# Optimization experiments

Measured on AMD Instinct MI355X. Metric: run time of the kernel, lower is better.

Reference implementation:

```python
import jax, jax.numpy as jnp
import numpy as np

B, C, NP, DM, H, TOPK = 16, 1024, 512, 512, 8, 16
D = DM // H  # d_head = 64


def _topk_mask(scores, k):
    """Binary mask keeping top-k entries per last-dim row. scores: (..., C)."""
    shape = scores.shape
    c = shape[-1]
    k = min(k, c)
    _, idx = jax.lax.top_k(scores, k)            # (..., k)
    flat = scores.reshape(-1, c)
    idxf = idx.reshape(-1, k)
    rows = jnp.arange(flat.shape[0])[:, None]
    mask = jnp.zeros_like(flat).at[rows, idxf].set(1.0)
    return mask.reshape(shape)


def setup_inputs() -> dict:
    key = jax.random.key(0)
    ks = jax.random.split(key, 7)
    M = jax.random.normal(ks[0], (B, C, NP), dtype=jnp.float32)
    s_in = 1.0 / np.sqrt(NP)
    Wq = jax.random.uniform(ks[1], (DM, NP), jnp.float32, -s_in, s_in)
    Wk = jax.random.uniform(ks[2], (DM, NP), jnp.float32, -s_in, s_in)
    Wv = jax.random.uniform(ks[3], (DM, NP), jnp.float32, -s_in, s_in)
    s_out = 1.0 / np.sqrt(DM)
    Wo = jax.random.uniform(ks[4], (NP, DM), jnp.float32, -s_out, s_out)
    bo = jax.random.uniform(ks[5], (NP,), jnp.float32, -s_out, s_out)
    gate = jnp.asarray(1.0, dtype=jnp.float32)
    return {"M": M, "Wq": Wq, "Wk": Wk, "Wv": Wv, "Wo": Wo, "bo": bo, "gate": gate}


def reference(M, Wq, Wk, Wv, Wo, bo, gate):
    # projections: torch Linear(no bias) -> M @ W.T
    def proj(W):
        x = jnp.einsum('bcn,dn->bcd', M, W)          # (B, C, DM)
        return x.reshape(B, C, H, D).transpose(0, 2, 1, 3)  # (B, H, C, D)

    q, k, v = proj(Wq), proj(Wk), proj(Wv)
    scale = D ** -0.5
    scores = jnp.einsum('bhid,bhjd->bhij', q, k) * scale     # (B, H, C, C)

    sparse_mask = jax.lax.stop_gradient(_topk_mask(scores, TOPK))
    neg_inf = jnp.finfo(scores.dtype).min
    masked = jnp.where(sparse_mask == 0, neg_inf, scores)
    attn = jnp.nan_to_num(jax.nn.softmax(masked, axis=-1))

    out = jnp.einsum('bhij,bhjd->bhid', attn, v)             # (B, H, C, D)
    out = out.transpose(0, 2, 1, 3).reshape(B, C, DM)        # (B, C, DM)
    delta = out @ Wo.T + bo                                  # (B, C, NP); dropout is eval-mode identity
    M_tilde = M + gate * delta

    avg_scores = scores.mean(axis=1)                         # (B, C, C)
    A = _topk_mask(avg_scores, TOPK)
    return M_tilde, A
```

## Files before the change

kernel.cpp:

```cpp
#include <hip/hip_runtime.h>
#include <hip/hip_bf16.h>

#define B_  16
#define C_  1024
#define NP_ 512
#define DM_ 512
#define H_  8
#define D_  64
#define BC_ 16384

#define PAVG_STRIDE 17
#define NBMAX 4
#define FLDS 40
#define FLDS2 72
#define STR_C 132

typedef unsigned long long ull;
typedef unsigned short u16;
using short8 = __attribute__((ext_vector_type(8))) short;
using half8  = __attribute__((ext_vector_type(8))) _Float16;
using f32x4  = __attribute__((ext_vector_type(4))) float;

__device__ __forceinline__ u16 f2bf(float x) {
    __hip_bfloat16 h = __float2bfloat16(x);
    return *reinterpret_cast<u16*>(&h);
}
__device__ __forceinline__ float bf2f(u16 v) {
    return __uint_as_float(((unsigned)v) << 16);
}
__device__ __forceinline__ u16 h_bits(_Float16 h) {
    return *reinterpret_cast<u16*>(&h);
}


__device__ __forceinline__ void hsplit_stage(const u16* __restrict__ Ah, const u16* __restrict__ Al,
    const u16* __restrict__ Bh, const u16* __restrict__ Bl,
    int lda, int ldb, int row0, int col0, int k0,
    u16* __restrict__ sAh, u16* __restrict__ sAl,
    u16* __restrict__ sBh, u16* __restrict__ sBl, int tid)
{
#pragma unroll
    for (int rep = 0; rep < 2; ++rep) {
        const int c = tid + rep * 256;
        const int row = c >> 2, kq = (c & 3) * 8;
        const size_t ga = (size_t)(row0 + row) * lda + k0 + kq;
        const size_t gb = (size_t)(col0 + row) * ldb + k0 + kq;
        *(uint4*)(&sAh[row * FLDS + kq]) = *(const uint4*)(Ah + ga);
        *(uint4*)(&sAl[row * FLDS + kq]) = *(const uint4*)(Al + ga);
        *(uint4*)(&sBh[row * FLDS + kq]) = *(const uint4*)(Bh + gb);
        *(uint4*)(&sBl[row * FLDS + kq]) = *(const uint4*)(Bl + gb);
    }
}

__device__ __forceinline__ void hsplit_compute(const u16* __restrict__ sAh, const u16* __restrict__ sAl,
    const u16* __restrict__ sBh, const u16* __restrict__ sBl,
    int lane, int wm, int wn, f32x4 (&acc)[4][4])
{
    const int q8 = (lane >> 4) * 8, l16 = lane & 15;
    half8 bh[4], bl_[4];
#pragma unroll
    for (int nt = 0; nt < 4; ++nt) {
        const int o = (wn * 64 + nt * 16 + l16) * FLDS + q8;
        bh[nt]  = *(const half8*)(&sBh[o]);
        bl_[nt] = *(const half8*)(&sBl[o]);
    }
#pragma unroll
    for (int mt = 0; mt < 4; ++mt) {
        const int o = (wm * 64 + mt * 16 + l16) * FLDS + q8;
        const half8 ah = *(const half8*)(&sAh[o]);
        const half8 al = *(const half8*)(&sAl[o]);
#pragma unroll
        for (int nt = 0; nt < 4; ++nt) {
            acc[mt][nt] = __builtin_amdgcn_mfma_f32_16x16x32_f16(ah, bh[nt],  acc[mt][nt], 0, 0, 0);
            acc[mt][nt] = __builtin_amdgcn_mfma_f32_16x16x32_f16(al, bh[nt],  acc[mt][nt], 0, 0, 0);
            acc[mt][nt] = __builtin_amdgcn_mfma_f32_16x16x32_f16(ah, bl_[nt], acc[mt][nt], 0, 0, 0);
            acc[mt][nt] = __builtin_amdgcn_mfma_f32_16x16x32_f16(al, bl_[nt], acc[mt][nt], 0, 0, 0);
        }
    }
}


__global__ __launch_bounds__(256) void w_convert(
    const float* __restrict__ Wo, const float* __restrict__ Wv,
    const float* __restrict__ Wq, const float* __restrict__ Wk,
    u16* __restrict__ Wob, u16* __restrict__ Wvb,
    u16* __restrict__ Wqh, u16* __restrict__ Wql,
    u16* __restrict__ Wkh, u16* __restrict__ Wkl)
{
    const int i = (blockIdx.x * 256 + threadIdx.x) * 4;
    const int y = blockIdx.y;
    if (y < 2) {
        const float* X = (y == 0) ? Wo : Wv;
        u16* Dp = (y == 0) ? Wob : Wvb;
        const float4 v = *(const float4*)(X + i);
        ushort4 o;
        o.x = f2bf(v.x); o.y = f2bf(v.y); o.z = f2bf(v.z); o.w = f2bf(v.w);
        *(ushort4*)(Dp + i) = o;
    } else {
        const float* X = (y == 2) ? Wq : Wk;
        u16* Hh = (y == 2) ? Wqh : Wkh;
        u16* Hl = (y == 2) ? Wql : Wkl;
        const float4 v = *(const float4*)(X + i);
        ushort4 oh, ol;
        {
            _Float16 h = (_Float16)v.x; oh.x = h_bits(h); ol.x = h_bits((_Float16)(v.x - (float)h));
        }{
            _Float16 h = (_Float16)v.y; oh.y = h_bits(h); ol.y = h_bits((_Float16)(v.y - (float)h));
        }{
            _Float16 h = (_Float16)v.z; oh.z = h_bits(h); ol.z = h_bits((_Float16)(v.z - (float)h));
        }{
            _Float16 h = (_Float16)v.w; oh.w = h_bits(h); ol.w = h_bits((_Float16)(v.w - (float)h));
        }
        *(ushort4*)(Hh + i) = oh;
        *(ushort4*)(Hl + i) = ol;
    }
}

__global__ __launch_bounds__(256) void mi_convert(const float* __restrict__ X,
    u16* __restrict__ Bb, u16* __restrict__ Hh, u16* __restrict__ Hl)
{
    const int i = (blockIdx.x * 256 + threadIdx.x) * 4;
    const float4 v = *(const float4*)(X + i);
    ushort4 ob, oh, ol;
    {
        _Float16 h = (_Float16)v.x; ob.x = f2bf(v.x); oh.x = h_bits(h); ol.x = h_bits((_Float16)(v.x - (float)h));
    }{
        _Float16 h = (_Float16)v.y; ob.y = f2bf(v.y); oh.y = h_bits(h); ol.y = h_bits((_Float16)(v.y - (float)h));
    }{
        _Float16 h = (_Float16)v.z; ob.z = f2bf(v.z); oh.z = h_bits(h); ol.z = h_bits((_Float16)(v.z - (float)h));
    }{
        _Float16 h = (_Float16)v.w; ob.w = f2bf(v.w); oh.w = h_bits(h); ol.w = h_bits((_Float16)(v.w - (float)h));
    }
    *(ushort4*)(Bb + i) = ob;
    *(ushort4*)(Hh + i) = oh;
    *(ushort4*)(Hl + i) = ol;
}

__global__ __launch_bounds__(256) void qk_gemm_mfma(
    const u16* __restrict__ Mih, const u16* __restrict__ Mil,
    const u16* __restrict__ Wqh, const u16* __restrict__ Wql,
    const u16* __restrict__ Wkh, const u16* __restrict__ Wkl,
    u16* __restrict__ Qh, u16* __restrict__ Ql,
    u16* __restrict__ Kh, u16* __restrict__ Kl)
{
    __shared__ u16 sAh[128 * FLDS];
    __shared__ u16 sAl[128 * FLDS];
    __shared__ u16 sBh[128 * FLDS];
    __shared__ u16 sBl[128 * FLDS];

    const int tid = threadIdx.x, lane = tid & 63, w = tid >> 6;
    const int wm = w >> 1, wn = w & 1;
    const int z = blockIdx.z;
    const u16* Bh = z ? Wkh : Wqh;
    const u16* Bl = z ? Wkl : Wql;
    u16* outH = z ? Kh : Qh;
    u16* outL = z ? Kl : Ql;
    const int row0 = blockIdx.x * 128, col0 = blockIdx.y * 128;

    f32x4 acc[4][4];
#pragma unroll
    for (int mt = 0; mt < 4; ++mt)
#pragma unroll
        for (int nt = 0; nt < 4; ++nt)
            acc[mt][nt] = (f32x4){0.f, 0.f, 0.f, 0.f};

    for (int k0 = 0; k0 < NP_; k0 += 32) {
        hsplit_stage(Mih, Mil, Bh, Bl, NP_, NP_, row0, col0, k0, sAh, sAl, sBh, sBl, tid);
        __syncthreads();
        hsplit_compute(sAh, sAl, sBh, sBl, lane, wm, wn, acc);
        __syncthreads();
    }

    const int quad = lane >> 4, l16 = lane & 15;
#pragma unroll
    for (int mt = 0; mt < 4; ++mt)
#pragma unroll
        for (int nt = 0; nt < 4; ++nt) {
            const int n = col0 + wn * 64 + nt * 16 + l16;
            const int hh = n >> 6, dd = n & 63;
#pragma unroll
            for (int reg = 0; reg < 4; ++reg) {
                const int m = row0 + wm * 64 + mt * 16 + quad * 4 + reg;
                const int bl = m >> 10, c = m & 1023;
                const size_t idx = ((size_t)(bl * 8 + hh) * C_ + c) * D_ + dd;
                const float v = acc[mt][nt][reg];
                const _Float16 vh = (_Float16)v;
                outH[idx] = h_bits(vh);
                outL[idx] = h_bits((_Float16)(v - (float)vh));
            }
        }
}

__global__ __launch_bounds__(256) void score_gemm_mfma(
    const u16* __restrict__ Qh, const u16* __restrict__ Ql,
    const u16* __restrict__ Kh, const u16* __restrict__ Kl,
    float* __restrict__ S)
{
    __shared__ u16 smem[4 * 128 * FLDS2];
    u16* sAh = smem;
    u16* sAl = smem + 128 * FLDS2;
    u16* sBh = smem + 2 * 128 * FLDS2;
    u16* sBl = smem + 3 * 128 * FLDS2;

    const int tid = threadIdx.x, lane = tid & 63, w = tid >> 6;
    const int wm = w >> 1, wn = w & 1;
    const int z = blockIdx.z;
    const size_t off = (size_t)z * C_ * D_;
    const u16* Ah = Qh + off;  const u16* Al = Ql + off;
    const u16* Bh = Kh + off;  const u16* Bl = Kl + off;
    float* Cp = S + (size_t)z * C_ * C_;
    const int row0 = blockIdx.x * 128, col0 = blockIdx.y * 128;

    f32x4 acc[4][4];
#pragma unroll
    for (int mt = 0; mt < 4; ++mt)
#pragma unroll
        for (int nt = 0; nt < 4; ++nt)
            acc[mt][nt] = (f32x4){0.f, 0.f, 0.f, 0.f};

#pragma unroll
    for (int rep = 0; rep < 4; ++rep) {
        const int c = tid + rep * 256;
        const int row = c >> 3, kq = (c & 7) * 8;
        const size_t ga = (size_t)(row0 + row) * D_ + kq;
        const size_t gb = (size_t)(col0 + row) * D_ + kq;
        *(uint4*)(&sAh[row * FLDS2 + kq]) = *(const uint4*)(Ah + ga);
        *(uint4*)(&sAl[row * FLDS2 + kq]) = *(const uint4*)(Al + ga);
        *(uint4*)(&sBh[row * FLDS2 + kq]) = *(const uint4*)(Bh + gb);
        *(uint4*)(&sBl[row * FLDS2 + kq]) = *(const uint4*)(Bl + gb);
    }
    __syncthreads();

    const int q8 = (lane >> 4) * 8, l16 = lane & 15;
#pragma unroll
    for (int ks = 0; ks < 2; ++ks) {
        const int kof = ks * 32 + q8;
        half8 bh[4], bl_[4];
#pragma unroll
        for (int nt = 0; nt < 4; ++nt) {
            const int o = (wn * 64 + nt * 16 + l16) * FLDS2 + kof;
            bh[nt]  = *(const half8*)(&sBh[o]);
            bl_[nt] = *(const half8*)(&sBl[o]);
        }
#pragma unroll
        for (int mt = 0; mt < 4; ++mt) {
            const int o = (wm * 64 + mt * 16 + l16) * FLDS2 + kof;
            const half8 ah = *(const half8*)(&sAh[o]);
            const half8 al = *(const half8*)(&sAl[o]);
#pragma unroll
            for (int nt = 0; nt < 4; ++nt) {
                acc[mt][nt] = __builtin_amdgcn_mfma_f32_16x16x32_f16(ah, bh[nt],  acc[mt][nt], 0, 0, 0);
                acc[mt][nt] = __builtin_amdgcn_mfma_f32_16x16x32_f16(al, bh[nt],  acc[mt][nt], 0, 0, 0);
                acc[mt][nt] = __builtin_amdgcn_mfma_f32_16x16x32_f16(ah, bl_[nt], acc[mt][nt], 0, 0, 0);
                acc[mt][nt] = __builtin_amdgcn_mfma_f32_16x16x32_f16(al, bl_[nt], acc[mt][nt], 0, 0, 0);
            }
        }
    }

    __syncthreads();
    float* st = (float*)smem;
    const int quad = lane >> 4;
#pragma unroll
    for (int mt = 0; mt < 4; ++mt)
#pragma unroll
        for (int nt = 0; nt < 4; ++nt) {
            const int n = wn * 64 + nt * 16 + l16;
#pragma unroll
            for (int reg = 0; reg < 4; ++reg) {
                const int m = wm * 64 + mt * 16 + quad * 4 + reg;
                st[m * STR_C + n] = acc[mt][nt][reg] * 0.125f;
            }
        }
    __syncthreads();
#pragma unroll
    for (int pass = 0; pass < 16; ++pass) {
        const int idx = pass * 256 + tid;
        const int row = idx >> 5;
        const int c4  = (idx & 31) << 2;
        const float4 v = *(const float4*)&st[row * STR_C + c4];
        *(float4*)(Cp + (size_t)(row0 + row) * C_ + col0 + c4) = v;
    }
}

__global__ __launch_bounds__(256) void v_gemm_mfma(const u16* __restrict__ Mib,
    const u16* __restrict__ Wvb, u16* __restrict__ Vb)
{
    __shared__ u16 As[128 * FLDS];
    __shared__ u16 Bs[128 * FLDS];
    const int tid = threadIdx.x, lane = tid & 63, w = tid >> 6;
    const int wm = w >> 1, wn = w & 1;
    const int row0 = blockIdx.x * 128, col0 = blockIdx.y * 128;

    f32x4 acc[4][4];
#pragma unroll
    for (int mt = 0; mt < 4; ++mt)
#pragma unroll
        for (int nt = 0; nt < 4; ++nt)
            acc[mt][nt] = (f32x4){0.f, 0.f, 0.f, 0.f};

    const int q8 = (lane >> 4) * 8, l16 = lane & 15;
    for (int k0 = 0; k0 < NP_; k0 += 32) {
#pragma unroll
        for (int rep = 0; rep < 2; ++rep) {
            const int c = tid + rep * 256;
            const int row = c >> 2, kq = (c & 3) * 8;
            *(uint4*)(&As[row * FLDS + kq]) = *(const uint4*)(Mib + (size_t)(row0 + row) * NP_ + k0 + kq);
            *(uint4*)(&Bs[row * FLDS + kq]) = *(const uint4*)(Wvb + (size_t)(col0 + row) * NP_ + k0 + kq);
        }
        __syncthreads();
        short8 a[4], bfr[4];
#pragma unroll
        for (int mt = 0; mt < 4; ++mt)
            a[mt] = *(const short8*)(&As[(wm * 64 + mt * 16 + l16) * FLDS + q8]);
#pragma unroll
        for (int nt = 0; nt < 4; ++nt)
            bfr[nt] = *(const short8*)(&Bs[(wn * 64 + nt * 16 + l16) * FLDS + q8]);
#pragma unroll
        for (int mt = 0; mt < 4; ++mt)
#pragma unroll
            for (int nt = 0; nt < 4; ++nt)
                acc[mt][nt] = __builtin_amdgcn_mfma_f32_16x16x32_bf16(a[mt], bfr[nt], acc[mt][nt], 0, 0, 0);
        __syncthreads();
    }
    const int quad = lane >> 4;
#pragma unroll
    for (int mt = 0; mt < 4; ++mt)
#pragma unroll
        for (int nt = 0; nt < 4; ++nt) {
            const int n = col0 + wn * 64 + nt * 16 + l16;
#pragma unroll
            for (int reg = 0; reg < 4; ++reg) {
                const int m = row0 + wm * 64 + mt * 16 + quad * 4 + reg;
                Vb[(size_t)m * DM_ + n] = f2bf(acc[mt][nt][reg]);
            }
        }
}


__device__ __forceinline__ ull pack1(float f, int j) {
    unsigned b = __float_as_uint(f);
    unsigned u = b ^ ((unsigned)((int)b >> 31) | 0x80000000u);
    return ((ull)u << 32) | (unsigned)(1023 - j);
}
__device__ __forceinline__ float unpack_val(ull e) {
    unsigned u = (unsigned)(e >> 32);
    unsigned b = u ^ ((u & 0x80000000u) ? 0x80000000u : 0xFFFFFFFFu);
    return __uint_as_float(b);
}
__device__ __forceinline__ int unpack_j(ull e) {
    return 1023 - (int)(e & 0xFFFFFFFFu);
}
__device__ __forceinline__ unsigned mono32(float f) {
    unsigned b = __float_as_uint(f);
    return b ^ ((unsigned)((int)b >> 31) | 0x80000000u);
}
__device__ __forceinline__ float mono32_inv(unsigned u) {
    unsigned b = u ^ ((u & 0x80000000u) ? 0x80000000u : 0xFFFFFFFFu);
    return __uint_as_float(b);
}

__device__ __forceinline__ unsigned radix16_u32(unsigned k)
{
    unsigned p = 0u;
#pragma unroll
    for (int b = 31; b >= 12; --b) {
        const unsigned t = p | (1u << b);
        if (__popcll(__ballot(k >= t)) >= 16) p = t;
    }
    return p;
}

__device__ __forceinline__ void radix16_dual_u32(unsigned kA, unsigned kB,
                                                 unsigned &pA, unsigned &pB)
{
    pA = 0u; pB = 0u;
#pragma unroll
    for (int b = 31; b >= 12; --b) {
        const unsigned tA = pA | (1u << b);
        const unsigned tB = pB | (1u << b);
        const ull mA = __ballot(kA >= tA);
        const ull mB = __ballot(kB >= tB);
        if (__popcll(mA) >= 16) pA = tA;
        if (__popcll(mB) >= 16) pB = tB;
    }
}

__device__ __forceinline__ void topk16_fast(float (&f)[16], const int lane,
                                            ull* candw, ull (&out)[16])
{
    float mv = f[0];
#pragma unroll
    for (int r = 1; r < 16; ++r) mv = fmaxf(mv, f[r]);
    const float tau = mono32_inv(radix16_u32(mono32(mv)));

    unsigned msk = 0u;
#pragma unroll
    for (int r = 0; r < 16; ++r) msk |= (f[r] >= tau) ? (1u << r) : 0u;
    const int cnt = __popc(msk);
    int incl = cnt;
#pragma unroll
    for (int off = 1; off < 64; off <<= 1) {
        const int t = __shfl_up(incl, off);
        incl += (lane >= off) ? t : 0;
    }
    const int total = __shfl(incl, 63);

    if (total <= 64) {
        int ofs = incl - cnt;
        unsigned m = msk;
        while (m) {
            const int r = __ffs(m) - 1;
            m &= m - 1;
            candw[ofs++] = pack1(f[r], (lane << 4) + r);
        }
        ull e = candw[lane];
        if (lane >= total) e = 0ull;
        if (total <= 32) {
#pragma unroll
            for (int k = 2; k <= 32; k <<= 1) {
#pragma unroll
                for (int j = k >> 1; j > 0; j >>= 1) {
                    const ull p = __shfl_xor(e, j);
                    const bool kmax = ((lane & k) == 0) == ((lane & j) == 0);
                    if ((p > e) == kmax) e = p;
                }
            }
        } else {
#pragma unroll
            for (int k = 2; k <= 64; k <<= 1) {
#pragma unroll
                for (int j = k >> 1; j > 0; j >>= 1) {
                    const ull p = __shfl_xor(e, j);
                    const bool kmax = ((lane & k) == 0) == ((lane & j) == 0);
                    if ((p > e) == kmax) e = p;
                }
            }
        }
#pragma unroll
        for (int t = 0; t < 16; ++t) out[t] = __shfl(e, t);
    } else {
        for (int it = 0; it < 16; ++it) {
            float bv = f[0]; int bj = lane << 4;
#pragma unroll
            for (int r = 1; r < 16; ++r)
                if (f[r] > bv) { bv = f[r]; bj = (lane << 4) + r; }
#pragma unroll
            for (int off = 32; off >= 1; off >>= 1) {
                const float ov = __shfl_xor(bv, off);
                const int   oj = __shfl_xor(bj, off);
                if (ov > bv || (ov == bv && oj < bj)) { bv = ov; bj = oj; }
            }
            out[it] = pack1(bv, bj);
            if ((bj >> 4) == lane) f[bj & 15] = -3.402823466e38f;
        }
    }
}

__device__ __forceinline__ ull topk16_serial(float (&f)[16], const int lane)
{
    ull e = 0ull;
    for (int it = 0; it < 16; ++it) {
        float bv = f[0]; int bj = lane << 4;
#pragma unroll
        for (int r = 1; r < 16; ++r)
            if (f[r] > bv) { bv = f[r]; bj = (lane << 4) + r; }
#pragma unroll
        for (int off = 32; off >= 1; off >>= 1) {
            const float ov = __shfl_xor(bv, off);
            const int   oj = __shfl_xor(bj, off);
            if (ov > bv || (ov == bv && oj < bj)) { bv = ov; bj = oj; }
        }
        if (lane == it) e = pack1(bv, bj);
        if ((bj >> 4) == lane) f[bj & 15] = -3.402823466e38f;
    }
    return e;
}

__device__ __forceinline__ void topk16_dual(float (&fA)[16], float (&fB)[16],
                                            const int lane, ull* cwA, ull* cwB,
                                            ull &eA, ull &eB)
{
    float mA = fA[0], mB = fB[0];
#pragma unroll
    for (int r = 1; r < 16; ++r) { mA = fmaxf(mA, fA[r]); mB = fmaxf(mB, fB[r]); }
    unsigned pA, pB;
    radix16_dual_u32(mono32(mA), mono32(mB), pA, pB);
    const float tauA = mono32_inv(pA);
    const float tauB = mono32_inv(pB);

    unsigned mskA = 0u, mskB = 0u;
#pragma unroll
    for (int r = 0; r < 16; ++r) {
        mskA |= (fA[r] >= tauA) ? (1u << r) : 0u;
        mskB |= (fB[r] >= tauB) ? (1u << r) : 0u;
    }
    const int cntA = __popc(mskA), cntB = __popc(mskB);
    int inclA = cntA, inclB = cntB;
#pragma unroll
    for (int off = 1; off < 64; off <<= 1) {
        const int tA = __shfl_up(inclA, off);
        const int tB = __shfl_up(inclB, off);
        inclA += (lane >= off) ? tA : 0;
        inclB += (lane >= off) ? tB : 0;
    }
    const int totalA = __shfl(inclA, 63);
    const int totalB = __shfl(inclB, 63);

    if (totalA <= 64) {
        int ofs = inclA - cntA;
        unsigned m = mskA;
        while (m) {
            const int r = __ffs(m) - 1;
            m &= m - 1;
            cwA[ofs++] = pack1(fA[r], (lane << 4) + r);
        }
    }
    if (totalB <= 64) {
        int ofs = inclB - cntB;
        unsigned m = mskB;
        while (m) {
            const int r = __ffs(m) - 1;
            m &= m - 1;
            cwB[ofs++] = pack1(fB[r], (lane << 4) + r);
        }
    }
    eA = (totalA <= 64 && lane < totalA) ? cwA[lane] : 0ull;
    eB = (totalB <= 64 && lane < totalB) ? cwB[lane] : 0ull;
    if (totalA <= 32 && totalB <= 32) {
#pragma unroll
        for (int k = 2; k <= 32; k <<= 1) {
#pragma unroll
            for (int j = k >> 1; j > 0; j >>= 1) {
                const ull pAx = __shfl_xor(eA, j);
                const ull pBx = __shfl_xor(eB, j);
                const bool kmax = ((lane & k) == 0) == ((lane & j) == 0);
                if ((pAx > eA) == kmax) eA = pAx;
                if ((pBx > eB) == kmax) eB = pBx;
            }
        }
    } else {
#pragma unroll
        for (int k = 2; k <= 64; k <<= 1) {
#pragma unroll
            for (int j = k >> 1; j > 0; j >>= 1) {
                const ull pAx = __shfl_xor(eA, j);
                const ull pBx = __shfl_xor(eB, j);
                const bool kmax = ((lane & k) == 0) == ((lane & j) == 0);
                if ((pAx > eA) == kmax) eA = pAx;
                if ((pBx > eB) == kmax) eB = pBx;
            }
        }
    }
    if (totalA > 64) eA = topk16_serial(fA, lane);
    if (totalB > 64) eB = topk16_serial(fB, lane);
}

__device__ __forceinline__ void attn_out(const ull e, const u16* __restrict__ V,
                                         int bl, int i, int h, int lane,
                                         u16* __restrict__ O)
{
    float vals[16]; int jl[16];
#pragma unroll
    for (int t = 0; t < 16; ++t) {
        const ull et = __shfl(e, t);
        vals[t] = unpack_val(et);
        jl[t]   = unpack_j(et);
    }
    const float mx = vals[0];
    float wv[16];
    float Z = 0.0f;
#pragma unroll
    for (int t = 0; t < 16; ++t) { wv[t] = __expf(vals[t] - mx); Z += wv[t]; }
    const float inv = 1.0f / Z;
#pragma unroll
    for (int t = 0; t < 16; ++t) wv[t] *= inv;
    float o = 0.0f;
#pragma unroll
    for (int t = 0; t < 16; ++t)
        o = fmaf(wv[t], bf2f(V[((size_t)(bl * C_ + jl[t])) * DM_ + h * D_ + lane]), o);
    O[((size_t)(bl * C_ + i)) * DM_ + h * D_ + lane] = f2bf(o);
}

__global__ __launch_bounds__(320) void topk_attn(const float* __restrict__ S,
    const u16* __restrict__ V, u16* __restrict__ O,
    float* __restrict__ Aout, int b0)
{
    __shared__ float pavg[4 * 64 * PAVG_STRIDE];
    __shared__ ull   cand[4][2][64];
    __shared__ ull   candA[64];

    const int tid = threadIdx.x, lane = tid & 63, w = tid >> 6;
    const int rb = blockIdx.x, bl = rb >> 10, i = rb & 1023;
    const int b = b0 + bl;

    float f1[16], f2[16];
    if (w < 4) {
        const float* r1 = S + ((size_t)(bl * 8 + w) * C_ + i) * C_ + lane * 16;
        const float* r2 = S + ((size_t)(bl * 8 + w + 4) * C_ + i) * C_ + lane * 16;
#pragma unroll
        for (int q = 0; q < 4; ++q) {
            const float4 x = *(const float4*)(r1 + q * 4);
            f1[q * 4 + 0] = x.x; f1[q * 4 + 1] = x.y; f1[q * 4 + 2] = x.z; f1[q * 4 + 3] = x.w;
            const float4 y = *(const float4*)(r2 + q * 4);
            f2[q * 4 + 0] = y.x; f2[q * 4 + 1] = y.y; f2[q * 4 + 2] = y.z; f2[q * 4 + 3] = y.w;
        }
        float* pw = pavg + w * 64 * PAVG_STRIDE + lane * PAVG_STRIDE;
#pragma unroll
        for (int r = 0; r < 16; ++r) pw[r] = f1[r] + f2[r];
    }
    __syncthreads();

    if (w < 4) {
        ull eA, eB;
        topk16_dual(f1, f2, lane, cand[w][0], cand[w][1], eA, eB);
        attn_out(eA, V, bl, i, w,     lane, O);
        attn_out(eB, V, bl, i, w + 4, lane, O);
    } else {
        float fa[16];
#pragma unroll
        for (int r = 0; r < 16; ++r) {
            fa[r] = pavg[0 * 64 * PAVG_STRIDE + lane * PAVG_STRIDE + r]
                  + pavg[1 * 64 * PAVG_STRIDE + lane * PAVG_STRIDE + r]
                  + pavg[2 * 64 * PAVG_STRIDE + lane * PAVG_STRIDE + r]
                  + pavg[3 * 64 * PAVG_STRIDE + lane * PAVG_STRIDE + r];
        }
        ull top[16];
        topk16_fast(fa, lane, candA, top);
        unsigned mybits = 0u;
#pragma unroll
        for (int t = 0; t < 16; ++t) {
            const int j = unpack_j(top[t]);
            if ((j >> 4) == lane) mybits |= 1u << (j & 15);
        }
        float* arow = Aout + ((size_t)(b * C_ + i)) * C_ + lane * 16;
#pragma unroll
        for (int q = 0; q < 4; ++q) {
            float4 o4;
            o4.x = ((mybits >> (q * 4 + 0)) & 1u) ? 1.0f : 0.0f;
            o4.y = ((mybits >> (q * 4 + 1)) & 1u) ? 1.0f : 0.0f;
            o4.z = ((mybits >> (q * 4 + 2)) & 1u) ? 1.0f : 0.0f;
            o4.w = ((mybits >> (q * 4 + 3)) & 1u) ? 1.0f : 0.0f;
            *(float4*)(arow + q * 4) = o4;
        }
    }
}

__global__ __launch_bounds__(256) void final_gemm_mfma(const u16* __restrict__ O,
    const u16* __restrict__ Wob, const float* __restrict__ Mi,
    const float* __restrict__ bo, const float* __restrict__ gatep,
    float* __restrict__ out)
{
    __shared__ u16 As[128 * FLDS];
    __shared__ u16 Bs[128 * FLDS];
    const int tid = threadIdx.x, lane = tid & 63, w = tid >> 6;
    const int wm = w >> 1, wn = w & 1;
    const int row0 = blockIdx.x * 128, col0 = blockIdx.y * 128;

    f32x4 acc[4][4];
#pragma unroll
    for (int mt = 0; mt < 4; ++mt)
#pragma unroll
        for (int nt = 0; nt < 4; ++nt)
            acc[mt][nt] = (f32x4){0.f, 0.f, 0.f, 0.f};

    const int q8 = (lane >> 4) * 8, l16 = lane & 15;
    for (int k0 = 0; k0 < DM_; k0 += 32) {
#pragma unroll
        for (int rep = 0; rep < 2; ++rep) {
            const int c = tid + rep * 256;
            const int row = c >> 2, kq = (c & 3) * 8;
            *(uint4*)(&As[row * FLDS + kq]) = *(const uint4*)(O   + (size_t)(row0 + row) * DM_ + k0 + kq);
            *(uint4*)(&Bs[row * FLDS + kq]) = *(const uint4*)(Wob + (size_t)(col0 + row) * DM_ + k0 + kq);
        }
        __syncthreads();
        short8 a[4], bfr[4];
#pragma unroll
        for (int mt = 0; mt < 4; ++mt)
            a[mt] = *(const short8*)(&As[(wm * 64 + mt * 16 + l16) * FLDS + q8]);
#pragma unroll
        for (int nt = 0; nt < 4; ++nt)
            bfr[nt] = *(const short8*)(&Bs[(wn * 64 + nt * 16 + l16) * FLDS + q8]);
#pragma unroll
        for (int mt = 0; mt < 4; ++mt)
#pragma unroll
            for (int nt = 0; nt < 4; ++nt)
                acc[mt][nt] = __builtin_amdgcn_mfma_f32_16x16x32_bf16(a[mt], bfr[nt], acc[mt][nt], 0, 0, 0);
        __syncthreads();
    }

    const float g = gatep[0];
    const int quad = lane >> 4;
#pragma unroll
    for (int mt = 0; mt < 4; ++mt) {
#pragma unroll
        for (int nt = 0; nt < 4; ++nt) {
            const int n = col0 + wn * 64 + nt * 16 + l16;
            const float bon = bo[n];
#pragma unroll
            for (int reg = 0; reg < 4; ++reg) {
                const int m = row0 + wm * 64 + mt * 16 + quad * 4 + reg;
                out[(size_t)m * NP_ + n] = Mi[(size_t)m * NP_ + n] + g * (acc[mt][nt][reg] + bon);
            }
        }
    }
}

extern "C" void kernel_launch(void* const* d_in, const int* in_sizes, int n_in,
                              void* d_out, int out_size, void* d_ws, size_t ws_size,
                              hipStream_t stream)
{
    (void)in_sizes; (void)n_in; (void)out_size;
    const float* Mi   = (const float*)d_in[0];
    const float* Wq   = (const float*)d_in[1];
    const float* Wk   = (const float*)d_in[2];
    const float* Wv   = (const float*)d_in[3];
    const float* Wo   = (const float*)d_in[4];
    const float* bo   = (const float*)d_in[5];
    const float* gate = (const float*)d_in[6];
    float* out  = (float*)d_out;
    float* Aout = out + (size_t)BC_ * NP_;

    char* p = (char*)d_ws;
    const size_t SZ_W   = (size_t)NP_ * DM_ * 2;
    const size_t SZ_BIG = (size_t)BC_ * DM_ * 2;
    u16* Wob = (u16*)p; p += SZ_W;
    u16* Wvb = (u16*)p; p += SZ_W;
    u16* Wqh = (u16*)p; p += SZ_W;
    u16* Wql = (u16*)p; p += SZ_W;
    u16* Wkh = (u16*)p; p += SZ_W;
    u16* Wkl = (u16*)p; p += SZ_W;
    u16* Mib = (u16*)p; p += SZ_BIG;
    u16* Mih = (u16*)p; p += SZ_BIG;
    u16* Mil = (u16*)p; p += SZ_BIG;
    u16* Qh  = (u16*)p; p += SZ_BIG;
    u16* Ql  = (u16*)p; p += SZ_BIG;
    u16* Kh  = (u16*)p; p += SZ_BIG;
    u16* Kl  = (u16*)p; p += SZ_BIG;
    u16* Vb  = (u16*)p; p += SZ_BIG;
    u16* Of  = (u16*)p; p += SZ_BIG;
    float* Sc = (float*)p;

    const size_t fixed = 6 * SZ_W + 9 * SZ_BIG;
    const size_t chunk_bytes = (size_t)H_ * C_ * C_ * 4;
    size_t availB = (ws_size > fixed) ? (ws_size - fixed) : 0;
    int NB = (int)(availB / chunk_bytes);
    if (NB < 1) NB = 1;
    if (NB > NBMAX) NB = NBMAX;

    w_convert<<<dim3(NP_ * DM_ / 1024, 4), 256, 0, stream>>>(
        Wo, Wv, Wq, Wk, Wob, Wvb, Wqh, Wql, Wkh, Wkl);
    mi_convert<<<dim3((int)((size_t)BC_ * NP_ / 1024)), 256, 0, stream>>>(Mi, Mib, Mih, Mil);

    qk_gemm_mfma<<<dim3(BC_ / 128, DM_ / 128, 2), 256, 0, stream>>>(
        Mih, Mil, Wqh, Wql, Wkh, Wkl, Qh, Ql, Kh, Kl);
    v_gemm_mfma<<<dim3(BC_ / 128, DM_ / 128), 256, 0, stream>>>(Mib, Wvb, Vb);

    for (int b0 = 0; b0 < B_; b0 += NB) {
        const int nb = (B_ - b0 < NB) ? (B_ - b0) : NB;
        const size_t hoff = (size_t)b0 * H_ * C_ * D_;
        score_gemm_mfma<<<dim3(C_ / 128, C_ / 128, nb * 8), 256, 0, stream>>>(
            Qh + hoff, Ql + hoff, Kh + hoff, Kl + hoff, Sc);
        topk_attn<<<dim3(nb * C_), 320, 0, stream>>>(
            Sc, Vb + (size_t)b0 * C_ * DM_, Of + (size_t)b0 * C_ * DM_, Aout, b0);
    }

    final_gemm_mfma<<<dim3(BC_ / 128, NP_ / 128), 256, 0, stream>>>(
        Of, Wob, Mi, bo, gate, out);
}
```

Before: 599.3 us.

## Use one wavefront per head in topk_attn instead of dual-row waves

The top-k attention kernel now launches 9 wavefronts per row block (8 heads plus one for the averaged mask) instead of 5, with each head wave running a single-row top-k rather than the interleaved dual-row routine. The head-sum reduction moves entirely into the averaging wave, which now reads eight LDS slices. The softmax in attn_out is also restructured to avoid per-lane register arrays. This raises parallelism per block and shortens the per-wave dependency chain, at the cost of larger blocks, more LDS and less instruction-level parallelism within each wave.

```diff
diff --git a/kernel.cpp b/kernel.cpp
--- a/kernel.cpp
+++ b/kernel.cpp
@@ -347,6 +347,10 @@
     unsigned b = u ^ ((u & 0x80000000u) ? 0x80000000u : 0xFFFFFFFFu);
     return __uint_as_float(b);
 }
+__device__ __forceinline__ float unpack_val_u32(unsigned u) {
+    unsigned b = u ^ ((u & 0x80000000u) ? 0x80000000u : 0xFFFFFFFFu);
+    return __uint_as_float(b);
+}
 __device__ __forceinline__ int unpack_j(ull e) {
     return 1023 - (int)(e & 0xFFFFFFFFu);
 }
@@ -370,23 +374,27 @@
     return p;
 }
 
-__device__ __forceinline__ void radix16_dual_u32(unsigned kA, unsigned kB,
-                                                 unsigned &pA, unsigned &pB)
-{
-    pA = 0u; pB = 0u;
-#pragma unroll
-    for (int b = 31; b >= 12; --b) {
-        const unsigned tA = pA | (1u << b);
-        const unsigned tB = pB | (1u << b);
-        const ull mA = __ballot(kA >= tA);
-        const ull mB = __ballot(kB >= tB);
-        if (__popcll(mA) >= 16) pA = tA;
-        if (__popcll(mB) >= 16) pB = tB;
-    }
-}
-
-__device__ __forceinline__ void topk16_fast(float (&f)[16], const int lane,
-                                            ull* candw, ull (&out)[16])
+__device__ __forceinline__ ull topk16_serial(float (&f)[16], const int lane)
+{
+    ull e = 0ull;
+    for (int it = 0; it < 16; ++it) {
+        float bv = f[0]; int bj = lane << 4;
+#pragma unroll
+        for (int r = 1; r < 16; ++r)
+            if (f[r] > bv) { bv = f[r]; bj = (lane << 4) + r; }
+#pragma unroll
+        for (int off = 32; off >= 1; off >>= 1) {
+            const float ov = __shfl_xor(bv, off);
+            const int   oj = __shfl_xor(bj, off);
+            if (ov > bv || (ov == bv && oj < bj)) { bv = ov; bj = oj; }
+        }
+        if (lane == it) e = pack1(bv, bj);
+        if ((bj >> 4) == lane) f[bj & 15] = -3.402823466e38f;
+    }
+    return e;
+}
+
+__device__ __forceinline__ ull topk16_single(float (&f)[16], const int lane, ull* candw)
 {
     float mv = f[0];
 #pragma unroll
@@ -413,8 +421,7 @@
             m &= m - 1;
             candw[ofs++] = pack1(f[r], (lane << 4) + r);
         }
-        ull e = candw[lane];
-        if (lane >= total) e = 0ull;
+        ull e = (lane < total) ? candw[lane] : 0ull;
         if (total <= 32) {
 #pragma unroll
             for (int k = 2; k <= 32; k <<= 1) {
@@ -436,200 +443,76 @@
                 }
             }
         }
-#pragma unroll
-        for (int t = 0; t < 16; ++t) out[t] = __shfl(e, t);
-    } else {
-        for (int it = 0; it < 16; ++it) {
-            float bv = f[0]; int bj = lane << 4;
-#pragma unroll
-            for (int r = 1; r < 16; ++r)
-                if (f[r] > bv) { bv = f[r]; bj = (lane << 4) + r; }
-#pragma unroll
-            for (int off = 32; off >= 1; off >>= 1) {
-                const float ov = __shfl_xor(bv, off);
-                const int   oj = __shfl_xor(bj, off);
-                if (ov > bv || (ov == bv && oj < bj)) { bv = ov; bj = oj; }
-            }
-            out[it] = pack1(bv, bj);
-            if ((bj >> 4) == lane) f[bj & 15] = -3.402823466e38f;
-        }
-    }
-}
-
-__device__ __forceinline__ ull topk16_serial(float (&f)[16], const int lane)
-{
-    ull e = 0ull;
-    for (int it = 0; it < 16; ++it) {
-        float bv = f[0]; int bj = lane << 4;
-#pragma unroll
-        for (int r = 1; r < 16; ++r)
-            if (f[r] > bv) { bv = f[r]; bj = (lane << 4) + r; }
-#pragma unroll
-        for (int off = 32; off >= 1; off >>= 1) {
-            const float ov = __shfl_xor(bv, off);
-            const int   oj = __shfl_xor(bj, off);
-            if (ov > bv || (ov == bv && oj < bj)) { bv = ov; bj = oj; }
-        }
-        if (lane == it) e = pack1(bv, bj);
-        if ((bj >> 4) == lane) f[bj & 15] = -3.402823466e38f;
-    }
-    return e;
-}
-
-__device__ __forceinline__ void topk16_dual(float (&fA)[16], float (&fB)[16],
-                                            const int lane, ull* cwA, ull* cwB,
-                                            ull &eA, ull &eB)
-{
-    float mA = fA[0], mB = fB[0];
-#pragma unroll
-    for (int r = 1; r < 16; ++r) { mA = fmaxf(mA, fA[r]); mB = fmaxf(mB, fB[r]); }
-    unsigned pA, pB;
-    radix16_dual_u32(mono32(mA), mono32(mB), pA, pB);
-    const float tauA = mono32_inv(pA);
-    const float tauB = mono32_inv(pB);
-
-    unsigned mskA = 0u, mskB = 0u;
-#pragma unroll
-    for (int r = 0; r < 16; ++r) {
-        mskA |= (fA[r] >= tauA) ? (1u << r) : 0u;
-        mskB |= (fB[r] >= tauB) ? (1u << r) : 0u;
-    }
-    const int cntA = __popc(mskA), cntB = __popc(mskB);
-    int inclA = cntA, inclB = cntB;
-#pragma unroll
-    for (int off = 1; off < 64; off <<= 1) {
-        const int tA = __shfl_up(inclA, off);
-        const int tB = __shfl_up(inclB, off);
-        inclA += (lane >= off) ? tA : 0;
-        inclB += (lane >= off) ? tB : 0;
-    }
-    const int totalA = __shfl(inclA, 63);
-    const int totalB = __shfl(inclB, 63);
-
-    if (totalA <= 64) {
-        int ofs = inclA - cntA;
-        unsigned m = mskA;
-        while (m) {
-            const int r = __ffs(m) - 1;
-            m &= m - 1;
-            cwA[ofs++] = pack1(fA[r], (lane << 4) + r);
-        }
-    }
-    if (totalB <= 64) {
-        int ofs = inclB - cntB;
-        unsigned m = mskB;
-        while (m) {
-            const int r = __ffs(m) - 1;
-            m &= m - 1;
-            cwB[ofs++] = pack1(fB[r], (lane << 4) + r);
-        }
-    }
-    eA = (totalA <= 64 && lane < totalA) ? cwA[lane] : 0ull;
-    eB = (totalB <= 64 && lane < totalB) ? cwB[lane] : 0ull;
-    if (totalA <= 32 && totalB <= 32) {
-#pragma unroll
-        for (int k = 2; k <= 32; k <<= 1) {
-#pragma unroll
-            for (int j = k >> 1; j > 0; j >>= 1) {
-                const ull pAx = __shfl_xor(eA, j);
-                const ull pBx = __shfl_xor(eB, j);
-                const bool kmax = ((lane & k) == 0) == ((lane & j) == 0);
-                if ((pAx > eA) == kmax) eA = pAx;
-                if ((pBx > eB) == kmax) eB = pBx;
-            }
-        }
-    } else {
-#pragma unroll
-        for (int k = 2; k <= 64; k <<= 1) {
-#pragma unroll
-            for (int j = k >> 1; j > 0; j >>= 1) {
-                const ull pAx = __shfl_xor(eA, j);
-                const ull pBx = __shfl_xor(eB, j);
-                const bool kmax = ((lane & k) == 0) == ((lane & j) == 0);
-                if ((pAx > eA) == kmax) eA = pAx;
-                if ((pBx > eB) == kmax) eB = pBx;
-            }
-        }
-    }
-    if (totalA > 64) eA = topk16_serial(fA, lane);
-    if (totalB > 64) eB = topk16_serial(fB, lane);
+        return e;
+    }
+    return topk16_serial(f, lane);
 }
 
 __device__ __forceinline__ void attn_out(const ull e, const u16* __restrict__ V,
                                          int bl, int i, int h, int lane,
                                          u16* __restrict__ O)
 {
-    float vals[16]; int jl[16];
+    const int ehi = (int)(unsigned)(e >> 32);
+    const float mx = unpack_val_u32((unsigned)__shfl(ehi, 0));
+    float Z = 0.0f;
+#pragma unroll
+    for (int t = 0; t < 16; ++t)
+        Z += __expf(unpack_val_u32((unsigned)__shfl(ehi, t)) - mx);
+    const float inv = 1.0f / Z;
+    float o = 0.0f;
 #pragma unroll
     for (int t = 0; t < 16; ++t) {
         const ull et = __shfl(e, t);
-        vals[t] = unpack_val(et);
-        jl[t]   = unpack_j(et);
-    }
-    const float mx = vals[0];
-    float wv[16];
-    float Z = 0.0f;
-#pragma unroll
-    for (int t = 0; t < 16; ++t) { wv[t] = __expf(vals[t] - mx); Z += wv[t]; }
-    const float inv = 1.0f / Z;
-#pragma unroll
-    for (int t = 0; t < 16; ++t) wv[t] *= inv;
-    float o = 0.0f;
-#pragma unroll
-    for (int t = 0; t < 16; ++t)
-        o = fmaf(wv[t], bf2f(V[((size_t)(bl * C_ + jl[t])) * DM_ + h * D_ + lane]), o);
+        const float wv = __expf(unpack_val(et) - mx) * inv;
+        o = fmaf(wv, bf2f(V[((size_t)(bl * C_ + unpack_j(et))) * DM_ + h * D_ + lane]), o);
+    }
     O[((size_t)(bl * C_ + i)) * DM_ + h * D_ + lane] = f2bf(o);
 }
 
-__global__ __launch_bounds__(320) void topk_attn(const float* __restrict__ S,
+__global__ __launch_bounds__(576) void topk_attn(const float* __restrict__ S,
     const u16* __restrict__ V, u16* __restrict__ O,
     float* __restrict__ Aout, int b0)
 {
-    __shared__ float pavg[4 * 64 * PAVG_STRIDE];
-    __shared__ ull   cand[4][2][64];
-    __shared__ ull   candA[64];
+    __shared__ float pavg[8 * 64 * PAVG_STRIDE];
+    __shared__ ull   cand[9][64];
 
     const int tid = threadIdx.x, lane = tid & 63, w = tid >> 6;
     const int rb = blockIdx.x, bl = rb >> 10, i = rb & 1023;
     const int b = b0 + bl;
 
-    float f1[16], f2[16];
-    if (w < 4) {
+    float f[16];
+    if (w < 8) {
         const float* r1 = S + ((size_t)(bl * 8 + w) * C_ + i) * C_ + lane * 16;
-        const float* r2 = S + ((size_t)(bl * 8 + w + 4) * C_ + i) * C_ + lane * 16;
 #pragma unroll
         for (int q = 0; q < 4; ++q) {
             const float4 x = *(const float4*)(r1 + q * 4);
-            f1[q * 4 + 0] = x.x; f1[q * 4 + 1] = x.y; f1[q * 4 + 2] = x.z; f1[q * 4 + 3] = x.w;
-            const float4 y = *(const float4*)(r2 + q * 4);
-            f2[q * 4 + 0] = y.x; f2[q * 4 + 1] = y.y; f2[q * 4 + 2] = y.z; f2[q * 4 + 3] = y.w;
+            f[q * 4 + 0] = x.x; f[q * 4 + 1] = x.y; f[q * 4 + 2] = x.z; f[q * 4 + 3] = x.w;
         }
         float* pw = pavg + w * 64 * PAVG_STRIDE + lane * PAVG_STRIDE;
 #pragma unroll
-        for (int r = 0; r < 16; ++r) pw[r] = f1[r] + f2[r];
+        for (int r = 0; r < 16; ++r) pw[r] = f[r];
     }
     __syncthreads();
 
-    if (w < 4) {
-        ull eA, eB;
-        topk16_dual(f1, f2, lane, cand[w][0], cand[w][1], eA, eB);
-        attn_out(eA, V, bl, i, w,     lane, O);
-        attn_out(eB, V, bl, i, w + 4, lane, O);
+    if (w < 8) {
+        const ull e = topk16_single(f, lane, cand[w]);
+        attn_out(e, V, bl, i, w, lane, O);
     } else {
         float fa[16];
 #pragma unroll
         for (int r = 0; r < 16; ++r) {
-            fa[r] = pavg[0 * 64 * PAVG_STRIDE + lane * PAVG_STRIDE + r]
-                  + pavg[1 * 64 * PAVG_STRIDE + lane * PAVG_STRIDE + r]
-                  + pavg[2 * 64 * PAVG_STRIDE + lane * PAVG_STRIDE + r]
-                  + pavg[3 * 64 * PAVG_STRIDE + lane * PAVG_STRIDE + r];
-        }
-        ull top[16];
-        topk16_fast(fa, lane, candA, top);
+            const int o = lane * PAVG_STRIDE + r;
+            const float t0 = pavg[0 * 64 * PAVG_STRIDE + o] + pavg[4 * 64 * PAVG_STRIDE + o];
+            const float t1 = pavg[1 * 64 * PAVG_STRIDE + o] + pavg[5 * 64 * PAVG_STRIDE + o];
+            const float t2 = pavg[2 * 64 * PAVG_STRIDE + o] + pavg[6 * 64 * PAVG_STRIDE + o];
+            const float t3 = pavg[3 * 64 * PAVG_STRIDE + o] + pavg[7 * 64 * PAVG_STRIDE + o];
+            fa[r] = ((t0 + t1) + t2) + t3;
+        }
+        const ull e = topk16_single(fa, lane, cand[8]);
         unsigned mybits = 0u;
 #pragma unroll
         for (int t = 0; t < 16; ++t) {
-            const int j = unpack_j(top[t]);
+            const int j = unpack_j(__shfl(e, t));
             if ((j >> 4) == lane) mybits |= 1u << (j & 15);
         }
         float* arow = Aout + ((size_t)(b * C_ + i)) * C_ + lane * 16;
@@ -760,7 +643,7 @@
         const size_t hoff = (size_t)b0 * H_ * C_ * D_;
         score_gemm_mfma<<<dim3(C_ / 128, C_ / 128, nb * 8), 256, 0, stream>>>(
             Qh + hoff, Ql + hoff, Kh + hoff, Kl + hoff, Sc);
-        topk_attn<<<dim3(nb * C_), 320, 0, stream>>>(
+        topk_attn<<<dim3(nb * C_), 576, 0, stream>>>(
             Sc, Vb + (size_t)b0 * C_ * DM_, Of + (size_t)b0 * C_ * DM_, Aout, b0);
     }
 
```

After: 637.6 us. 1.06x slower.
